# Optimization experiments

Hardware: AMD Instinct MI355X
Metric: run time of the kernel (lower is better)

## Reference

```python
import jax, jax.numpy as jnp
import numpy as np

N, E = 50000, 800000
DIN, DOUT, DEDGE, HEADS = 128, 128, 64, 1


def setup_inputs() -> dict:
    key = jax.random.key(0)
    ks = jax.random.split(key, 16)
    s = 0.02
    inp = {
        "x": jax.random.normal(ks[0], (N, DIN), jnp.float32),
        "edge_index": jax.random.randint(ks[1], (2, E), 0, N, dtype=jnp.int32),
        "edge_attr": jax.random.normal(ks[2], (E, DEDGE), jnp.float32),
        # TransformerConv params (PyG defaults: q/k/v/skip have bias, lin_edge has no bias)
        "Wq": jax.random.normal(ks[3], (DIN, HEADS * DOUT), jnp.float32) * s,
        "bq": jnp.zeros((HEADS * DOUT,), jnp.float32),
        "Wk": jax.random.normal(ks[4], (DIN, HEADS * DOUT), jnp.float32) * s,
        "bk": jnp.zeros((HEADS * DOUT,), jnp.float32),
        "Wv": jax.random.normal(ks[5], (DIN, HEADS * DOUT), jnp.float32) * s,
        "bv": jnp.zeros((HEADS * DOUT,), jnp.float32),
        "We": jax.random.normal(ks[6], (DEDGE, HEADS * DOUT), jnp.float32) * s,
        "Wskip": jax.random.normal(ks[7], (DIN, HEADS * DOUT), jnp.float32) * s,
        "bskip": jnp.zeros((HEADS * DOUT,), jnp.float32),
        # LayerNorm
        "ln_g": jnp.ones((DOUT,), jnp.float32),
        "ln_b": jnp.zeros((DOUT,), jnp.float32),
        # GatedResidualConnection
        "Wres": jax.random.normal(ks[8], (DIN, DOUT), jnp.float32) * s,
        "bres": jnp.zeros((DOUT,), jnp.float32),
        "Wgate": jax.random.normal(ks[9], (DIN, 1), jnp.float32) * s,
        "bgate": jnp.zeros((1,), jnp.float32),
    }
    return inp


def _transformer_conv(x, edge_index, edge_attr, Wq, bq, Wk, bk, Wv, bv, We, Wskip, bskip):
    H, C = HEADS, DOUT
    src, dst = edge_index[0], edge_index[1]  # j -> i (aggregate at dst)
    q = (x @ Wq + bq).reshape(-1, H, C)
    k = (x @ Wk + bk).reshape(-1, H, C)
    v = (x @ Wv + bv).reshape(-1, H, C)
    e = (edge_attr @ We).reshape(-1, H, C)  # [E,H,C]
    k_j = k[src] + e
    v_j = v[src] + e
    q_i = q[dst]
    alpha = jnp.sum(q_i * k_j, axis=-1) / jnp.sqrt(jnp.float32(C))  # [E,H]
    # segment softmax over incoming edges of each dst node
    amax = jax.ops.segment_max(alpha, dst, num_segments=N)  # [N,H]
    ex = jnp.exp(alpha - amax[dst])
    denom = jax.ops.segment_sum(ex, dst, num_segments=N)  # [N,H]
    p = ex / denom[dst]  # [E,H]
    out = jax.ops.segment_sum(p[..., None] * v_j, dst, num_segments=N)  # [N,H,C]
    out = out.reshape(-1, H * C)
    out = out + (x @ Wskip + bskip)  # root weight skip
    return out


def reference(x, edge_index, edge_attr, Wq, bq, Wk, bk, Wv, bv, We, Wskip, bskip,
              ln_g, ln_b, Wres, bres, Wgate, bgate):
    out = _transformer_conv(x, edge_index, edge_attr, Wq, bq, Wk, bk, Wv, bv, We, Wskip, bskip)
    # LayerNorm(out_channels)
    mu = jnp.mean(out, axis=-1, keepdims=True)
    var = jnp.mean(jnp.square(out - mu), axis=-1, keepdims=True)
    out = (out - mu) / jnp.sqrt(var + 1e-5) * ln_g + ln_b
    out = jax.nn.relu(out)
    # gated residual
    residual = x @ Wres + bres
    gate = jax.nn.sigmoid(x @ Wgate + bgate)  # [N,1]
    return gate * out + (1.0 - gate) * residual
```

## Files before the change

kernel.cpp:

```cpp
#include <hip/hip_runtime.h>
#include <math.h>

#define NN 50000
#define EE 800000
#define NPAD 50048
#define PC 768

typedef short bf16x8 __attribute__((ext_vector_type(8)));
typedef float f32x4 __attribute__((ext_vector_type(4)));

#define ASCALE 0.08838834764831845f

__device__ inline short f2bf(float f)
{
    unsigned u = __float_as_uint(f);
    u = u + 0x7fff + ((u >> 16) & 1);
    return (short)(u >> 16);
}

__global__ __launch_bounds__(256) void k_wprep(const float* __restrict__ Wq,
                                               const float* __restrict__ bq,
                                               const float* __restrict__ We,
                                               float* __restrict__ wqe,
                                               float* __restrict__ bqe)
{
    int idx = blockIdx.x * 256 + threadIdx.x;
    if (idx < 8192) {
        int r = idx >> 6, m = idx & 63;
        float acc = 0.f;
        for (int c = 0; c < 128; ++c) acc += Wq[r * 128 + c] * We[m * 128 + c];
        wqe[r * 64 + m] = acc;
    } else if (idx < 8256) {
        int m = idx - 8192;
        float acc = 0.f;
        for (int c = 0; c < 128; ++c) acc += bq[c] * We[m * 128 + c];
        bqe[m] = acc;
    }
}

__global__ __launch_bounds__(256) void k_packx(const float* __restrict__ x,
                                               short* __restrict__ Xb)
{
    int t = blockIdx.x * 256 + threadIdx.x;
    int base = t * 4;
    if (base >= NPAD * 128) return;
    short s0 = 0, s1 = 0, s2 = 0, s3 = 0;
    if (base < NN * 128) {
        const float4 v = *(const float4*)(x + base);
        s0 = f2bf(v.x); s1 = f2bf(v.y); s2 = f2bf(v.z); s3 = f2bf(v.w);
    }
    short4 o; o.x = s0; o.y = s1; o.z = s2; o.w = s3;
    *(short4*)(Xb + base) = o;
}

__global__ __launch_bounds__(256) void k_packw(
    const float* __restrict__ Wq, const float* __restrict__ bq,
    const float* __restrict__ Wk, const float* __restrict__ bk,
    const float* __restrict__ Wv, const float* __restrict__ bv,
    const float* __restrict__ Wskip, const float* __restrict__ bskip,
    const float* __restrict__ Wres, const float* __restrict__ bres,
    const float* __restrict__ Wgate, const float* __restrict__ bgate,
    const float* __restrict__ wqe, const float* __restrict__ bqe,
    short* __restrict__ WT, float* __restrict__ bias)
{
    int idx = blockIdx.x * 256 + threadIdx.x;
    if (idx < PC * 128) {
        int col = idx >> 7, k = idx & 127;
        float v;
        if (col < 128)      v = Wq[k * 128 + col];
        else if (col < 256) v = Wk[k * 128 + (col - 128)];
        else if (col < 384) v = Wv[k * 128 + (col - 256)];
        else if (col < 512) v = Wskip[k * 128 + (col - 384)];
        else if (col < 640) v = Wres[k * 128 + (col - 512)];
        else if (col < 704) v = wqe[k * 64 + (col - 640)];
        else if (col == 704) v = Wgate[k];
        else                v = 0.f;
        WT[col * 128 + k] = f2bf(v);
    } else if (idx < PC * 128 + PC) {
        int col = idx - PC * 128;
        float b;
        if (col < 128)      b = bq[col];
        else if (col < 256) b = bk[col - 128];
        else if (col < 384) b = bv[col - 256];
        else if (col < 512) b = bskip[col - 384];
        else if (col < 640) b = bres[col - 512];
        else if (col < 704) b = bqe[col - 640];
        else if (col == 704) b = bgate[0];
        else                b = 0.f;
        bias[col] = b;
    }
}

#define LROW 136
__global__ __launch_bounds__(256) void k_gemm(const short* __restrict__ Xb,
                                              const short* __restrict__ WT,
                                              const float* __restrict__ bias,
                                              float* __restrict__ P)
{
    __shared__ short Al[128 * LROW];
    __shared__ short Bl[64 * LROW];

    int bm = blockIdx.x;
    int bn = blockIdx.y;
    int tid = threadIdx.x;

    const short* gA = Xb + (size_t)bm * 128 * 128;
    const short* gB = WT + (size_t)bn * 64 * 128;

#pragma unroll
    for (int it = 0; it < 8; ++it) {
        int g = it * 256 + tid;
        int row = g >> 4, c8 = g & 15;
        *(bf16x8*)&Al[row * LROW + c8 * 8] = *(const bf16x8*)(gA + g * 8);
    }
#pragma unroll
    for (int it = 0; it < 4; ++it) {
        int g = it * 256 + tid;
        int row = g >> 4, c8 = g & 15;
        *(bf16x8*)&Bl[row * LROW + c8 * 8] = *(const bf16x8*)(gB + g * 8);
    }
    __syncthreads();

    int wave = tid >> 6, lane = tid & 63;
    int quad = lane >> 4, l16 = lane & 15;
    int r0 = wave * 32;

    f32x4 acc[2][4] = {};
#pragma unroll
    for (int ks = 0; ks < 4; ++ks) {
        int k0 = ks * 32 + quad * 8;
        bf16x8 af0 = *(const bf16x8*)&Al[(r0 + l16) * LROW + k0];
        bf16x8 af1 = *(const bf16x8*)&Al[(r0 + 16 + l16) * LROW + k0];
#pragma unroll
        for (int cn = 0; cn < 4; ++cn) {
            bf16x8 bfr = *(const bf16x8*)&Bl[(cn * 16 + l16) * LROW + k0];
            acc[0][cn] = __builtin_amdgcn_mfma_f32_16x16x32_bf16(af0, bfr, acc[0][cn], 0, 0, 0);
            acc[1][cn] = __builtin_amdgcn_mfma_f32_16x16x32_bf16(af1, bfr, acc[1][cn], 0, 0, 0);
        }
    }

#pragma unroll
    for (int half = 0; half < 2; ++half) {
        int growb = bm * 128 + r0 + half * 16 + quad * 4;
#pragma unroll
        for (int cn = 0; cn < 4; ++cn) {
            int gcol = bn * 64 + cn * 16 + l16;
            float b = bias[gcol];
#pragma unroll
            for (int i = 0; i < 4; ++i) {
                int grow = growb + i;
                if (grow < NN) {
                    float v = acc[half][cn][i] + b;
                    if (gcol == 704) v = 1.f / (1.f + __expf(-v));
                    P[(size_t)grow * PC + gcol] = v;
                }
            }
        }
    }
}

__global__ __launch_bounds__(256) void k_hist(const int* __restrict__ ei,
                                              int* __restrict__ deg, int E)
{
    int e = blockIdx.x * 256 + threadIdx.x;
    if (e < E) atomicAdd(&deg[ei[E + e]], 1);
}

__global__ __launch_bounds__(256) void k_scan1(const int* __restrict__ deg,
                                               int* __restrict__ rs,
                                               int* __restrict__ cs, int n)
{
    __shared__ int sh[256];
    int base = blockIdx.x * 1024;
    int t = threadIdx.x;
    int idx = base + t * 4;
    int v[4];
#pragma unroll
    for (int k = 0; k < 4; ++k) v[k] = (idx + k < n) ? deg[idx + k] : 0;
    int sum = v[0] + v[1] + v[2] + v[3];
    sh[t] = sum;
    __syncthreads();
    for (int off = 1; off < 256; off <<= 1) {
        int add = (t >= off) ? sh[t - off] : 0;
        __syncthreads();
        sh[t] += add;
        __syncthreads();
    }
    int run = sh[t] - sum;
    if (t == 255) cs[blockIdx.x] = sh[255];
#pragma unroll
    for (int k = 0; k < 4; ++k) {
        if (idx + k < n) rs[idx + k] = run;
        run += v[k];
    }
}

__global__ void k_scan2(int* __restrict__ cs, int nc)
{
    __shared__ int sh[64];
    int t = threadIdx.x;
    sh[t] = (t < nc) ? cs[t] : 0;
    __syncthreads();
    if (t == 0) {
        int acc = 0;
        for (int i = 0; i < nc; ++i) { int v = sh[i]; sh[i] = acc; acc += v; }
    }
    __syncthreads();
    if (t < nc) cs[t] = sh[t];
}

__global__ __launch_bounds__(256) void k_scan3(int* __restrict__ rs,
                                               const int* __restrict__ cs,
                                               int* __restrict__ cur, int n, int E)
{
    int i = blockIdx.x * 256 + threadIdx.x;
    if (i < n) {
        int v = rs[i] + cs[i >> 10];
        rs[i] = v;
        cur[i] = v;
    } else if (i == n) {
        rs[n] = E;
    }
}

__global__ __launch_bounds__(256) void k_scatter(const int* __restrict__ ei,
                                                 int* __restrict__ cur,
                                                 int2* __restrict__ sj, int E)
{
    int e = blockIdx.x * 256 + threadIdx.x;
    if (e < E) {
        int d = ei[E + e];
        int pos = atomicAdd(&cur[d], 1);
        int2 v; v.x = ei[e]; v.y = e;
        sj[pos] = v;
    }
}

__device__ inline float wave_allreduce(float v)
{
    v += __shfl_xor(v, 32);
    v += __shfl_xor(v, 16);
    v += __shfl_xor(v, 8);
    v += __shfl_xor(v, 4);
    v += __shfl_xor(v, 2);
    v += __shfl_xor(v, 1);
    return v;
}

__global__ __launch_bounds__(256) void k_attn(
    const float* __restrict__ P, const float* __restrict__ ea,
    const int* __restrict__ rs, const int2* __restrict__ sj,
    float* __restrict__ T, float* __restrict__ S, float* __restrict__ denom,
    int n)
{
    int node = blockIdx.x * 4 + (threadIdx.x >> 6);
    int lane = threadIdx.x & 63;
    if (node >= n) return;

    const float* Prow = P + (size_t)node * PC;
    float q0 = Prow[lane];
    float q1 = Prow[64 + lane];
    float wq = Prow[640 + lane];

    float accd = 0.f, t0 = 0.f, t1 = 0.f, sA = 0.f;
    int beg = rs[node], end = rs[node + 1];

    int p = beg;
    for (; p + 4 <= end; p += 4) {
        int2 s0 = sj[p], s1 = sj[p + 1], s2 = sj[p + 2], s3 = sj[p + 3];
        const float* kv0 = P + (size_t)s0.x * PC + 128;
        const float* kv1 = P + (size_t)s1.x * PC + 128;
        const float* kv2 = P + (size_t)s2.x * PC + 128;
        const float* kv3 = P + (size_t)s3.x * PC + 128;
        const float* ar0 = ea + (size_t)s0.y * 64;
        const float* ar1 = ea + (size_t)s1.y * 64;
        const float* ar2 = ea + (size_t)s2.y * 64;
        const float* ar3 = ea + (size_t)s3.y * 64;

        float k00 = kv0[lane], k01 = kv0[64 + lane];
        float v00 = kv0[128 + lane], v01 = kv0[192 + lane];
        float k10 = kv1[lane], k11 = kv1[64 + lane];
        float v10 = kv1[128 + lane], v11 = kv1[192 + lane];
        float k20 = kv2[lane], k21 = kv2[64 + lane];
        float v20 = kv2[128 + lane], v21 = kv2[192 + lane];
        float k30 = kv3[lane], k31 = kv3[64 + lane];
        float v30 = kv3[128 + lane], v31 = kv3[192 + lane];
        float a0 = __builtin_nontemporal_load(ar0 + lane);
        float a1 = __builtin_nontemporal_load(ar1 + lane);
        float a2 = __builtin_nontemporal_load(ar2 + lane);
        float a3 = __builtin_nontemporal_load(ar3 + lane);

        float p0 = q0 * k00 + q1 * k01 + wq * a0;
        float p1 = q0 * k10 + q1 * k11 + wq * a1;
        float p2 = q0 * k20 + q1 * k21 + wq * a2;
        float p3 = q0 * k30 + q1 * k31 + wq * a3;

#pragma unroll
        for (int o = 32; o > 0; o >>= 1) {
            p0 += __shfl_xor(p0, o);
            p1 += __shfl_xor(p1, o);
            p2 += __shfl_xor(p2, o);
            p3 += __shfl_xor(p3, o);
        }

        float ex0 = __expf(p0 * ASCALE);
        float ex1 = __expf(p1 * ASCALE);
        float ex2 = __expf(p2 * ASCALE);
        float ex3 = __expf(p3 * ASCALE);

        accd += (ex0 + ex1) + (ex2 + ex3);
        t0 += ex0 * v00 + ex1 * v10 + ex2 * v20 + ex3 * v30;
        t1 += ex0 * v01 + ex1 * v11 + ex2 * v21 + ex3 * v31;
        sA += ex0 * a0 + ex1 * a1 + ex2 * a2 + ex3 * a3;
    }

    for (; p < end; ++p) {
        int2 s0 = sj[p];
        const float* kv = P + (size_t)s0.x * PC + 128;
        const float* ar = ea + (size_t)s0.y * 64;
        float k0 = kv[lane], k1 = kv[64 + lane];
        float v0 = kv[128 + lane], v1 = kv[192 + lane];
        float a = __builtin_nontemporal_load(ar + lane);
        float part = q0 * k0 + q1 * k1 + wq * a;
        float ex = __expf(wave_allreduce(part) * ASCALE);
        accd += ex;
        t0 += ex * v0;
        t1 += ex * v1;
        sA += ex * a;
    }

    T[(size_t)node * 128 + lane] = t0;
    T[(size_t)node * 128 + 64 + lane] = t1;
    S[(size_t)node * 64 + lane] = sA;
    if (lane == 0) denom[node] = accd;
}

__global__ __launch_bounds__(256) void k_final(
    const float* __restrict__ T, const float* __restrict__ S,
    const float* __restrict__ denom, const float* __restrict__ P,
    const float* __restrict__ We, const float* __restrict__ ln_g,
    const float* __restrict__ ln_b, float* __restrict__ out, int n)
{
    __shared__ float sWe[64 * 128];
    for (int i = threadIdx.x; i < 64 * 128; i += 256) sWe[i] = We[i];
    __syncthreads();

    int node = blockIdx.x * 4 + (threadIdx.x >> 6);
    int lane = threadIdx.x & 63;
    if (node >= n) return;

    const float* Prow = P + (size_t)node * PC;

    float sv = S[(size_t)node * 64 + lane];
    float a0 = T[(size_t)node * 128 + lane];
    float a1 = T[(size_t)node * 128 + 64 + lane];
#pragma unroll 16
    for (int m = 0; m < 64; ++m) {
        float sm = __shfl(sv, m);
        a0 += sm * sWe[m * 128 + lane];
        a1 += sm * sWe[m * 128 + 64 + lane];
    }

    float d = denom[node];
    float rcp = d > 0.f ? 1.f / d : 0.f;
    a0 = a0 * rcp + Prow[384 + lane];
    a1 = a1 * rcp + Prow[448 + lane];

    float s = wave_allreduce(a0 + a1);
    float mean = s * (1.f / 128.f);
    float d0 = a0 - mean, d1 = a1 - mean;
    float vs = wave_allreduce(d0 * d0 + d1 * d1);
    float inv = rsqrtf(vs * (1.f / 128.f) + 1e-5f);
    float n0 = d0 * inv * ln_g[lane] + ln_b[lane];
    float n1 = d1 * inv * ln_g[64 + lane] + ln_b[64 + lane];
    n0 = fmaxf(n0, 0.f);
    n1 = fmaxf(n1, 0.f);

    float g = Prow[704];
    float r0 = Prow[512 + lane];
    float r1 = Prow[576 + lane];
    out[(size_t)node * 128 + lane] = g * n0 + (1.f - g) * r0;
    out[(size_t)node * 128 + 64 + lane] = g * n1 + (1.f - g) * r1;
}

extern "C" void kernel_launch(void* const* d_in, const int* in_sizes, int n_in,
                              void* d_out, int out_size, void* d_ws, size_t ws_size,
                              hipStream_t stream)
{
    const float* x     = (const float*)d_in[0];
    const int*   ei    = (const int*)d_in[1];
    const float* ea    = (const float*)d_in[2];
    const float* Wq    = (const float*)d_in[3];
    const float* bq    = (const float*)d_in[4];
    const float* Wk    = (const float*)d_in[5];
    const float* bk    = (const float*)d_in[6];
    const float* Wv    = (const float*)d_in[7];
    const float* bv    = (const float*)d_in[8];
    const float* We    = (const float*)d_in[9];
    const float* Wskip = (const float*)d_in[10];
    const float* bskip = (const float*)d_in[11];
    const float* ln_g  = (const float*)d_in[12];
    const float* ln_b  = (const float*)d_in[13];
    const float* Wres  = (const float*)d_in[14];
    const float* bres  = (const float*)d_in[15];
    const float* Wgate = (const float*)d_in[16];
    const float* bgate = (const float*)d_in[17];
    float* out = (float*)d_out;

    float* W = (float*)d_ws;
    size_t o = 0;
    auto falloc = [&](size_t e) { size_t r = o; o += e; return r; };
    size_t oP    = falloc((size_t)NN * PC);
    size_t oT    = falloc((size_t)NN * 128);
    size_t oS    = falloc((size_t)NN * 64);
    size_t oDEN  = falloc(NN);
    size_t oWQE  = falloc(8192);
    size_t oBQE  = falloc(64);
    size_t oBIAS = falloc(PC);

    short* SB = (short*)(W + o);
    size_t oXB = 0;
    size_t oWT = oXB + (size_t)NPAD * 128;
    size_t sh_total = oWT + (size_t)PC * 128;

    int* IB = (int*)(SB + ((sh_total + 1) & ~(size_t)1));
    size_t io = 0;
    auto ialloc = [&](size_t e) { size_t r = io; io += e; return r; };
    size_t oSJ   = ialloc((size_t)2 * EE);
    size_t oDEG  = ialloc(NN);
    size_t oRS   = ialloc(NN + 1);
    size_t oCUR  = ialloc(NN);
    size_t oCS   = ialloc(64);

    hipMemsetAsync(IB + oDEG, 0, NN * sizeof(int), stream);

    k_wprep<<<33, 256, 0, stream>>>(Wq, bq, We, W + oWQE, W + oBQE);
    k_packx<<<(NPAD * 128 / 4 + 255) / 256, 256, 0, stream>>>(x, SB + oXB);
    k_packw<<<(PC * 128 + PC + 255) / 256, 256, 0, stream>>>(
        Wq, bq, Wk, bk, Wv, bv, Wskip, bskip, Wres, bres, Wgate, bgate,
        W + oWQE, W + oBQE, SB + oWT, W + oBIAS);

    dim3 ggrid(NPAD / 128, PC / 64);
    k_gemm<<<ggrid, 256, 0, stream>>>(SB + oXB, SB + oWT, W + oBIAS, W + oP);

    k_hist<<<(EE + 255) / 256, 256, 0, stream>>>(ei, IB + oDEG, EE);
    k_scan1<<<49, 256, 0, stream>>>(IB + oDEG, IB + oRS, IB + oCS, NN);
    k_scan2<<<1, 64, 0, stream>>>(IB + oCS, 49);
    k_scan3<<<(NN + 256) / 256, 256, 0, stream>>>(IB + oRS, IB + oCS, IB + oCUR, NN, EE);
    k_scatter<<<(EE + 255) / 256, 256, 0, stream>>>(ei, IB + oCUR, (int2*)(IB + oSJ), EE);

    k_attn<<<NN / 4, 256, 0, stream>>>(W + oP, ea, IB + oRS, (const int2*)(IB + oSJ),
                                       W + oT, W + oS, W + oDEN, NN);

    k_final<<<NN / 4, 256, 0, stream>>>(W + oT, W + oS, W + oDEN, W + oP,
                                        We, ln_g, ln_b, out, NN);
}
```

Before: 655.9 us.

## Fuse attention and finalize kernels, store K/V as packed bf16

```diff
diff --git a/kernel.cpp b/kernel.cpp
--- a/kernel.cpp
+++ b/kernel.cpp
@@ -11,11 +11,11 @@
 
 #define ASCALE 0.08838834764831845f
 
-__device__ inline short f2bf(float f)
+__device__ inline unsigned short f2bf(float f)
 {
     unsigned u = __float_as_uint(f);
     u = u + 0x7fff + ((u >> 16) & 1);
-    return (short)(u >> 16);
+    return (unsigned short)(u >> 16);
 }
 
 __global__ __launch_bounds__(256) void k_wprep(const float* __restrict__ Wq,
@@ -61,7 +61,9 @@
     const float* __restrict__ Wres, const float* __restrict__ bres,
     const float* __restrict__ Wgate, const float* __restrict__ bgate,
     const float* __restrict__ wqe, const float* __restrict__ bqe,
-    short* __restrict__ WT, float* __restrict__ bias)
+    const float* __restrict__ We,
+    short* __restrict__ WT, float* __restrict__ bias,
+    unsigned short* __restrict__ WeTb)
 {
     int idx = blockIdx.x * 256 + threadIdx.x;
     if (idx < PC * 128) {
@@ -75,7 +77,7 @@
         else if (col < 704) v = wqe[k * 64 + (col - 640)];
         else if (col == 704) v = Wgate[k];
         else                v = 0.f;
-        WT[col * 128 + k] = f2bf(v);
+        WT[col * 128 + k] = (short)f2bf(v);
     } else if (idx < PC * 128 + PC) {
         int col = idx - PC * 128;
         float b;
@@ -88,6 +90,10 @@
         else if (col == 704) b = bgate[0];
         else                b = 0.f;
         bias[col] = b;
+    } else if (idx < PC * 128 + PC + 128 * 72) {
+        int i2 = idx - (PC * 128 + PC);
+        int c = i2 / 72, kk = i2 % 72;
+        WeTb[i2] = (kk < 64) ? f2bf(We[kk * 128 + c]) : (unsigned short)0;
     }
 }
 
@@ -95,13 +101,14 @@
 __global__ __launch_bounds__(256) void k_gemm(const short* __restrict__ Xb,
                                               const short* __restrict__ WT,
                                               const float* __restrict__ bias,
-                                              float* __restrict__ P)
+                                              float* __restrict__ P,
+                                              unsigned short* __restrict__ KVb16)
 {
     __shared__ short Al[128 * LROW];
     __shared__ short Bl[64 * LROW];
 
-    int bm = blockIdx.x;
-    int bn = blockIdx.y;
+    int bn = blockIdx.x;
+    int bm = blockIdx.y;
     int tid = threadIdx.x;
 
     const short* gA = Xb + (size_t)bm * 128 * 128;
@@ -139,6 +146,7 @@
         }
     }
 
+    bool isKV = (bn >= 2 && bn <= 5);
 #pragma unroll
     for (int half = 0; half < 2; ++half) {
         int growb = bm * 128 + r0 + half * 16 + quad * 4;
@@ -151,8 +159,17 @@
                 int grow = growb + i;
                 if (grow < NN) {
                     float v = acc[half][cn][i] + b;
-                    if (gcol == 704) v = 1.f / (1.f + __expf(-v));
-                    P[(size_t)grow * PC + gcol] = v;
+                    if (isKV) {
+                        int slot;
+                        if (gcol < 192)      slot = (gcol - 128) * 2;
+                        else if (gcol < 256) slot = (gcol - 192) * 2 + 1;
+                        else if (gcol < 320) slot = 128 + (gcol - 256) * 2;
+                        else                 slot = 128 + (gcol - 320) * 2 + 1;
+                        KVb16[(size_t)grow * 256 + slot] = f2bf(v);
+                    } else {
+                        if (gcol == 704) v = 1.f / (1.f + __expf(-v));
+                        P[(size_t)grow * PC + gcol] = v;
+                    }
                 }
             }
         }
@@ -236,26 +253,26 @@
     }
 }
 
-__device__ inline float wave_allreduce(float v)
-{
-    v += __shfl_xor(v, 32);
-    v += __shfl_xor(v, 16);
-    v += __shfl_xor(v, 8);
-    v += __shfl_xor(v, 4);
-    v += __shfl_xor(v, 2);
-    v += __shfl_xor(v, 1);
-    return v;
-}
-
-__global__ __launch_bounds__(256) void k_attn(
-    const float* __restrict__ P, const float* __restrict__ ea,
+__global__ __launch_bounds__(256) void k_attn_fused(
+    const float* __restrict__ P, const unsigned int* __restrict__ KVb,
+    const float* __restrict__ ea, const unsigned short* __restrict__ WeTb,
     const int* __restrict__ rs, const int2* __restrict__ sj,
-    float* __restrict__ T, float* __restrict__ S, float* __restrict__ denom,
-    int n)
-{
-    int node = blockIdx.x * 4 + (threadIdx.x >> 6);
-    int lane = threadIdx.x & 63;
-    if (node >= n) return;
+    const float* __restrict__ ln_g, const float* __restrict__ ln_b,
+    float* __restrict__ out)
+{
+    __shared__ unsigned short WeT_l[128 * 72];
+    __shared__ unsigned short Sb_l[4 * 64];
+    __shared__ float att_l[4 * 128];
+
+    int tid = threadIdx.x;
+    {
+        const unsigned int* src = (const unsigned int*)WeTb;
+        unsigned int* dst = (unsigned int*)WeT_l;
+        for (int i = tid; i < 128 * 36; i += 256) dst[i] = src[i];
+    }
+
+    int wave = tid >> 6, lane = tid & 63;
+    int node = blockIdx.x * 4 + wave;
 
     const float* Prow = P + (size_t)node * PC;
     float q0 = Prow[lane];
@@ -266,110 +283,95 @@
     int beg = rs[node], end = rs[node + 1];
 
     int p = beg;
-    for (; p + 4 <= end; p += 4) {
-        int2 s0 = sj[p], s1 = sj[p + 1], s2 = sj[p + 2], s3 = sj[p + 3];
-        const float* kv0 = P + (size_t)s0.x * PC + 128;
-        const float* kv1 = P + (size_t)s1.x * PC + 128;
-        const float* kv2 = P + (size_t)s2.x * PC + 128;
-        const float* kv3 = P + (size_t)s3.x * PC + 128;
-        const float* ar0 = ea + (size_t)s0.y * 64;
-        const float* ar1 = ea + (size_t)s1.y * 64;
-        const float* ar2 = ea + (size_t)s2.y * 64;
-        const float* ar3 = ea + (size_t)s3.y * 64;
-
-        float k00 = kv0[lane], k01 = kv0[64 + lane];
-        float v00 = kv0[128 + lane], v01 = kv0[192 + lane];
-        float k10 = kv1[lane], k11 = kv1[64 + lane];
-        float v10 = kv1[128 + lane], v11 = kv1[192 + lane];
-        float k20 = kv2[lane], k21 = kv2[64 + lane];
-        float v20 = kv2[128 + lane], v21 = kv2[192 + lane];
-        float k30 = kv3[lane], k31 = kv3[64 + lane];
-        float v30 = kv3[128 + lane], v31 = kv3[192 + lane];
-        float a0 = __builtin_nontemporal_load(ar0 + lane);
-        float a1 = __builtin_nontemporal_load(ar1 + lane);
-        float a2 = __builtin_nontemporal_load(ar2 + lane);
-        float a3 = __builtin_nontemporal_load(ar3 + lane);
-
-        float p0 = q0 * k00 + q1 * k01 + wq * a0;
-        float p1 = q0 * k10 + q1 * k11 + wq * a1;
-        float p2 = q0 * k20 + q1 * k21 + wq * a2;
-        float p3 = q0 * k30 + q1 * k31 + wq * a3;
-
+    for (; p + 8 <= end; p += 8) {
+        float pp[8], aa[8], v0[8], v1[8];
+#pragma unroll
+        for (int u = 0; u < 8; ++u) {
+            int2 s = sj[p + u];
+            const unsigned int* kv = KVb + (size_t)s.x * 128;
+            unsigned int kw = kv[lane];
+            unsigned int vw = kv[64 + lane];
+            float a = __builtin_nontemporal_load(ea + (size_t)s.y * 64 + lane);
+            float k0 = __uint_as_float(kw << 16);
+            float k1 = __uint_as_float(kw & 0xffff0000u);
+            v0[u] = __uint_as_float(vw << 16);
+            v1[u] = __uint_as_float(vw & 0xffff0000u);
+            aa[u] = a;
+            pp[u] = q0 * k0 + q1 * k1 + wq * a;
+        }
 #pragma unroll
         for (int o = 32; o > 0; o >>= 1) {
-            p0 += __shfl_xor(p0, o);
-            p1 += __shfl_xor(p1, o);
-            p2 += __shfl_xor(p2, o);
-            p3 += __shfl_xor(p3, o);
-        }
-
-        float ex0 = __expf(p0 * ASCALE);
-        float ex1 = __expf(p1 * ASCALE);
-        float ex2 = __expf(p2 * ASCALE);
-        float ex3 = __expf(p3 * ASCALE);
-
-        accd += (ex0 + ex1) + (ex2 + ex3);
-        t0 += ex0 * v00 + ex1 * v10 + ex2 * v20 + ex3 * v30;
-        t1 += ex0 * v01 + ex1 * v11 + ex2 * v21 + ex3 * v31;
-        sA += ex0 * a0 + ex1 * a1 + ex2 * a2 + ex3 * a3;
-    }
-
+#pragma unroll
+            for (int u = 0; u < 8; ++u) pp[u] += __shfl_xor(pp[u], o);
+        }
+#pragma unroll
+        for (int u = 0; u < 8; ++u) {
+            float ex = __expf(pp[u] * ASCALE);
+            accd += ex;
+            t0 += ex * v0[u];
+            t1 += ex * v1[u];
+            sA += ex * aa[u];
+        }
+    }
     for (; p < end; ++p) {
-        int2 s0 = sj[p];
-        const float* kv = P + (size_t)s0.x * PC + 128;
-        const float* ar = ea + (size_t)s0.y * 64;
-        float k0 = kv[lane], k1 = kv[64 + lane];
-        float v0 = kv[128 + lane], v1 = kv[192 + lane];
-        float a = __builtin_nontemporal_load(ar + lane);
+        int2 s = sj[p];
+        const unsigned int* kv = KVb + (size_t)s.x * 128;
+        unsigned int kw = kv[lane];
+        unsigned int vw = kv[64 + lane];
+        float a = __builtin_nontemporal_load(ea + (size_t)s.y * 64 + lane);
+        float k0 = __uint_as_float(kw << 16);
+        float k1 = __uint_as_float(kw & 0xffff0000u);
+        float vv0 = __uint_as_float(vw << 16);
+        float vv1 = __uint_as_float(vw & 0xffff0000u);
         float part = q0 * k0 + q1 * k1 + wq * a;
-        float ex = __expf(wave_allreduce(part) * ASCALE);
+#pragma unroll
+        for (int o = 32; o > 0; o >>= 1) part += __shfl_xor(part, o);
+        float ex = __expf(part * ASCALE);
         accd += ex;
-        t0 += ex * v0;
-        t1 += ex * v1;
+        t0 += ex * vv0;
+        t1 += ex * vv1;
         sA += ex * a;
     }
 
-    T[(size_t)node * 128 + lane] = t0;
-    T[(size_t)node * 128 + 64 + lane] = t1;
-    S[(size_t)node * 64 + lane] = sA;
-    if (lane == 0) denom[node] = accd;
-}
-
-__global__ __launch_bounds__(256) void k_final(
-    const float* __restrict__ T, const float* __restrict__ S,
-    const float* __restrict__ denom, const float* __restrict__ P,
-    const float* __restrict__ We, const float* __restrict__ ln_g,
-    const float* __restrict__ ln_b, float* __restrict__ out, int n)
-{
-    __shared__ float sWe[64 * 128];
-    for (int i = threadIdx.x; i < 64 * 128; i += 256) sWe[i] = We[i];
-    __syncthreads();
-
-    int node = blockIdx.x * 4 + (threadIdx.x >> 6);
-    int lane = threadIdx.x & 63;
-    if (node >= n) return;
-
-    const float* Prow = P + (size_t)node * PC;
-
-    float sv = S[(size_t)node * 64 + lane];
-    float a0 = T[(size_t)node * 128 + lane];
-    float a1 = T[(size_t)node * 128 + 64 + lane];
-#pragma unroll 16
-    for (int m = 0; m < 64; ++m) {
-        float sm = __shfl(sv, m);
-        a0 += sm * sWe[m * 128 + lane];
-        a1 += sm * sWe[m * 128 + 64 + lane];
-    }
-
-    float d = denom[node];
-    float rcp = d > 0.f ? 1.f / d : 0.f;
-    a0 = a0 * rcp + Prow[384 + lane];
-    a1 = a1 * rcp + Prow[448 + lane];
-
-    float s = wave_allreduce(a0 + a1);
+
+    Sb_l[wave * 64 + lane] = f2bf(sA);
+    __syncthreads();
+
+    {
+        int quad = lane >> 4, l16 = lane & 15;
+        int arow = l16 & 3;
+        bf16x8 a0 = *(const bf16x8*)&Sb_l[arow * 64 + quad * 8];
+        bf16x8 a1 = *(const bf16x8*)&Sb_l[arow * 64 + 32 + quad * 8];
+#pragma unroll
+        for (int c2 = 0; c2 < 2; ++c2) {
+            int cn = wave * 2 + c2;
+            int r = cn * 16 + l16;
+            bf16x8 b0 = *(const bf16x8*)&WeT_l[r * 72 + quad * 8];
+            bf16x8 b1 = *(const bf16x8*)&WeT_l[r * 72 + 32 + quad * 8];
+            f32x4 acc = {};
+            acc = __builtin_amdgcn_mfma_f32_16x16x32_bf16(a0, b0, acc, 0, 0, 0);
+            acc = __builtin_amdgcn_mfma_f32_16x16x32_bf16(a1, b1, acc, 0, 0, 0);
+            if (quad == 0) {
+#pragma unroll
+                for (int i = 0; i < 4; ++i)
+                    att_l[i * 128 + cn * 16 + l16] = acc[i];
+            }
+        }
+    }
+    __syncthreads();
+
+    float rcp = accd > 0.f ? 1.f / accd : 0.f;
+    float a0f = (t0 + att_l[wave * 128 + lane]) * rcp + Prow[384 + lane];
+    float a1f = (t1 + att_l[wave * 128 + 64 + lane]) * rcp + Prow[448 + lane];
+
+    float s = a0f + a1f;
+#pragma unroll
+    for (int o = 32; o > 0; o >>= 1) s += __shfl_xor(s, o);
     float mean = s * (1.f / 128.f);
-    float d0 = a0 - mean, d1 = a1 - mean;
-    float vs = wave_allreduce(d0 * d0 + d1 * d1);
+    float d0 = a0f - mean, d1 = a1f - mean;
+    float vs = d0 * d0 + d1 * d1;
+#pragma unroll
+    for (int o = 32; o > 0; o >>= 1) vs += __shfl_xor(vs, o);
     float inv = rsqrtf(vs * (1.f / 128.f) + 1e-5f);
     float n0 = d0 * inv * ln_g[lane] + ln_b[lane];
     float n1 = d1 * inv * ln_g[64 + lane] + ln_b[64 + lane];
@@ -411,17 +413,16 @@
     size_t o = 0;
     auto falloc = [&](size_t e) { size_t r = o; o += e; return r; };
     size_t oP    = falloc((size_t)NN * PC);
-    size_t oT    = falloc((size_t)NN * 128);
-    size_t oS    = falloc((size_t)NN * 64);
-    size_t oDEN  = falloc(NN);
     size_t oWQE  = falloc(8192);
     size_t oBQE  = falloc(64);
     size_t oBIAS = falloc(PC);
+    size_t oKVB  = falloc((size_t)NN * 128);
 
     short* SB = (short*)(W + o);
-    size_t oXB = 0;
-    size_t oWT = oXB + (size_t)NPAD * 128;
-    size_t sh_total = oWT + (size_t)PC * 128;
+    size_t oXB  = 0;
+    size_t oWT  = oXB + (size_t)NPAD * 128;
+    size_t oWET = oWT + (size_t)PC * 128;
+    size_t sh_total = oWET + 128 * 72;
 
     int* IB = (int*)(SB + ((sh_total + 1) & ~(size_t)1));
     size_t io = 0;
@@ -436,12 +437,14 @@
 
     k_wprep<<<33, 256, 0, stream>>>(Wq, bq, We, W + oWQE, W + oBQE);
     k_packx<<<(NPAD * 128 / 4 + 255) / 256, 256, 0, stream>>>(x, SB + oXB);
-    k_packw<<<(PC * 128 + PC + 255) / 256, 256, 0, stream>>>(
+    k_packw<<<(PC * 128 + PC + 128 * 72 + 255) / 256, 256, 0, stream>>>(
         Wq, bq, Wk, bk, Wv, bv, Wskip, bskip, Wres, bres, Wgate, bgate,
-        W + oWQE, W + oBQE, SB + oWT, W + oBIAS);
-
-    dim3 ggrid(NPAD / 128, PC / 64);
-    k_gemm<<<ggrid, 256, 0, stream>>>(SB + oXB, SB + oWT, W + oBIAS, W + oP);
+        W + oWQE, W + oBQE, We, SB + oWT, W + oBIAS,
+        (unsigned short*)(SB + oWET));
+
+    dim3 ggrid(PC / 64, NPAD / 128);
+    k_gemm<<<ggrid, 256, 0, stream>>>(SB + oXB, SB + oWT, W + oBIAS, W + oP,
+                                      (unsigned short*)(W + oKVB));
 
     k_hist<<<(EE + 255) / 256, 256, 0, stream>>>(ei, IB + oDEG, EE);
     k_scan1<<<49, 256, 0, stream>>>(IB + oDEG, IB + oRS, IB + oCS, NN);
@@ -449,9 +452,8 @@
     k_scan3<<<(NN + 256) / 256, 256, 0, stream>>>(IB + oRS, IB + oCS, IB + oCUR, NN, EE);
     k_scatter<<<(EE + 255) / 256, 256, 0, stream>>>(ei, IB + oCUR, (int2*)(IB + oSJ), EE);
 
-    k_attn<<<NN / 4, 256, 0, stream>>>(W + oP, ea, IB + oRS, (const int2*)(IB + oSJ),
-                                       W + oT, W + oS, W + oDEN, NN);
-
-    k_final<<<NN / 4, 256, 0, stream>>>(W + oT, W + oS, W + oDEN, W + oP,
-                                        We, ln_g, ln_b, out, NN);
-}
+    k_attn_fused<<<NN / 4, 256, 0, stream>>>(
+        W + oP, (const unsigned int*)(W + oKVB), ea,
+        (const unsigned short*)(SB + oWET),
+        IB + oRS, (const int2*)(IB + oSJ), ln_g, ln_b, out);
+}
```

Measured after the change: 589.5 us. 10.1% less time.
